# Kernel optimization log

Hardware: AMD Instinct MI355X
Metric: run time of the kernel (lower is better)

The kernel has to match this reference:

```python
import jax, jax.numpy as jnp
import numpy as np

B, N = 256, 64          # molecules, atoms per molecule
EMB = 64                # atom embedding dim
G = 64                  # n_gaussians
HID = 128               # interaction hidden
OUT = 512               # output_dim
GAUSS_WIDTH = 0.5


def setup_inputs() -> dict:
    key = jax.random.key(0)
    ks = jax.random.split(key, 10)
    atomic_nums = jax.random.randint(ks[0], (B, N), 0, 120, dtype=jnp.int64 if jax.config.x64_enabled else jnp.int32)
    coords = jax.random.normal(ks[1], (B, N, 3), dtype=jnp.float32) * 3.0
    embed_table = jax.random.normal(ks[2], (120, EMB), dtype=jnp.float32)
    # interaction: Linear(128->128), GELU, Linear(128->128); weights stored (in, out)
    W1 = jax.random.normal(ks[3], (EMB + G, HID), dtype=jnp.float32) / np.sqrt(EMB + G)
    b1 = jnp.zeros((HID,), dtype=jnp.float32)
    W2 = jax.random.normal(ks[4], (HID, HID), dtype=jnp.float32) / np.sqrt(HID)
    b2 = jnp.zeros((HID,), dtype=jnp.float32)
    # output_proj: Linear(128 -> 512)
    Wo = jax.random.normal(ks[5], (HID, OUT), dtype=jnp.float32) / np.sqrt(HID)
    bo = jnp.zeros((OUT,), dtype=jnp.float32)
    centers = jnp.linspace(0.0, 10.0, G).astype(jnp.float32)
    return {"atomic_nums": atomic_nums, "coords": coords, "embed_table": embed_table,
            "W1": W1, "b1": b1, "W2": W2, "b2": b2, "Wo": Wo, "bo": bo, "centers": centers}


def reference(atomic_nums, coords, embed_table, W1, b1, W2, b2, Wo, bo, centers):
    # per-atom embedding: [B,N,EMB]
    emb = embed_table[atomic_nums]
    # pairwise distances: [B,N,N]; guard sqrt(0) for diagonal
    diff = coords[:, :, None, :] - coords[:, None, :, :]
    sq = jnp.sum(diff * diff, axis=-1)
    pos = sq > 0
    dists = jnp.where(pos, jnp.sqrt(jnp.where(pos, sq, 1.0)), 0.0)
    # Gaussian smearing: [B,N,N,G]
    gauss = jnp.exp(-0.5 * jnp.square((dists[..., None] - centers) / GAUSS_WIDTH))
    # mean over neighbor axis j: [B,N,G]
    avg_gauss = gauss.mean(axis=2)
    feat = jnp.concatenate([emb, avg_gauss], axis=-1)  # [B,N,EMB+G]
    h = jax.nn.gelu(feat @ W1 + b1, approximate=False) @ W2 + b2  # [B,N,HID]
    mol = h.mean(axis=1)  # [B,HID]
    return mol @ Wo + bo  # [B,OUT]
```

## Files before the change

### kernel.cpp

```cpp
#include <hip/hip_runtime.h>
#include <math.h>

namespace {
constexpr int NB   = 256;
constexpr int NA   = 64;
constexpr int EMBD = 64;
constexpr int HIDD = 128;
constexpr int OUTD = 512;
constexpr int FPS  = 136;
constexpr int DSTR = 68;

typedef __attribute__((ext_vector_type(8))) short bfrag8;
typedef __attribute__((ext_vector_type(4))) float floatx4;

__device__ __forceinline__ unsigned short bf16_rne(float f) {
    unsigned u = __float_as_uint(f);
    u += 0x7fffu + ((u >> 16) & 1u);
    return (unsigned short)(u >> 16);
}

__device__ __forceinline__ float gelu_fast(float x) {
    const float ax = fabsf(x) * 0.7071067811865475f;
    const float t  = __builtin_amdgcn_rcpf(fmaf(0.3275911f, ax, 1.0f));
    float p = fmaf(1.061405429f, t, -1.453152027f);
    p = fmaf(p, t, 1.421413741f);
    p = fmaf(p, t, -0.284496736f);
    p = fmaf(p, t, 0.254829592f);
    p = p * t;
    const float e = __builtin_amdgcn_exp2f(-1.4426950408889634f * ax * ax);
    const float erfx = copysignf(fmaf(-p, e, 1.0f), x);
    const float hx   = 0.5f * x;
    return fmaf(hx, erfx, hx);
}


__global__ __launch_bounds__(1024, 1)
void mlip_fused(const int*   __restrict__ atomic_nums,
                const float* __restrict__ coords,
                const float* __restrict__ embed_table,
                const float* __restrict__ W1, const float* __restrict__ b1,
                const float* __restrict__ W2, const float* __restrict__ b2,
                const float* __restrict__ Wo, const float* __restrict__ bo,
                const float* __restrict__ centers,
                float*       __restrict__ out)
{
    const int b    = blockIdx.x;
    const int tid  = threadIdx.x;
    const int lane = tid & 63;
    const int wid  = tid >> 6;

    __shared__ float s_dist[NA * DSTR];
    __shared__ short s_w[16384];
    __shared__ short s_fhi[NA][FPS], s_flo[NA][FPS];
    __shared__ float s_mol[4][HIDD];
    __shared__ float s_molv[HIDD];

    const int wm      = wid & 3, wn = wid >> 2;
    const int lrow    = lane & 15, g4 = lane >> 4;
    const int arow    = (wm << 4) + lrow;
    const int colbase = (wn << 5) + lrow;

    const int gcol = tid & 127, kc = tid >> 7;
    const int colT = tid >> 1, kh = tid & 1;

    const int grow = tid >> 4;
    const int gch  = (tid >> 2) & 3;
    const int jq   = tid & 3;

    const float bo_r = bo[colT];
    const float b1a  = b1[colbase];
    const float b1b  = b1[colbase + 16];
    const float b2r  = b2[gcol];
    const float c0   = centers[gch << 4];

    float w1v[16];
#pragma unroll
    for (int a = 0; a < 2; ++a) {
        const int slot = (a << 10) + tid;
        const int fg = slot >> 6, ls = slot & 63;
        const int k0 = ((fg >> 3) << 5) + ((ls >> 4) << 3);
        const int n  = ((fg & 7) << 4) + (ls & 15);
        const float* src = W1 + (size_t)k0 * HIDD + n;
#pragma unroll
        for (int r = 0; r < 8; ++r) w1v[a * 8 + r] = src[(size_t)r * HIDD];
    }

    const float* cbase = coords + (size_t)b * NA * 3;
    const float cx = cbase[lane * 3 + 0];
    const float cy = cbase[lane * 3 + 1];
    const float cz = cbase[lane * 3 + 2];
    {
        const int i = tid >> 4, e4 = (tid & 15) << 2;
        const int z = atomic_nums[b * NA + i];
        const float4 ev = *(const float4*)(embed_table + (size_t)z * EMBD + e4);
        short4 h4, l4;
        const float v[4] = {ev.x, ev.y, ev.z, ev.w};
        short* hp = (short*)&h4; short* lp = (short*)&l4;
#pragma unroll
        for (int q = 0; q < 4; ++q) {
            const unsigned short h = bf16_rne(v[q]);
            hp[q] = (short)h;
            lp[q] = (short)bf16_rne(v[q] - __uint_as_float((unsigned)h << 16));
        }
        *(short4*)&s_fhi[i][e4] = h4;
        *(short4*)&s_flo[i][e4] = l4;
    }

#pragma unroll
    for (int it = 0; it < 4; ++it) {
        const int i = (wid << 2) + it;
        const float xi = __shfl(cx, i, 64);
        const float yi = __shfl(cy, i, 64);
        const float zi = __shfl(cz, i, 64);
        const float dx = xi - cx, dy = yi - cy, dz = zi - cz;
        const float sq = dx * dx + dy * dy + dz * dz;
        s_dist[i * DSTR + lane] = sq > 0.0f ? sqrtf(sq) : 0.0f;
    }

#pragma unroll
    for (int a = 0; a < 2; ++a) {
        unsigned Hu[4];
#pragma unroll
        for (int p = 0; p < 4; ++p) {
            const float x = w1v[a * 8 + 2 * p], y = w1v[a * 8 + 2 * p + 1];
            unsigned h;
            asm("v_cvt_pk_bf16_f32 %0, %1, %2" : "=v"(h) : "v"(x), "v"(y));
            Hu[p] = h;
        }
        const int slot = (a << 10) + tid;
        const int base = ((slot >> 6) << 9) + (slot & 63) * 8;
        *(uint4*)&s_w[base] = make_uint4(Hu[0], Hu[1], Hu[2], Hu[3]);
    }

    {
        constexpr float L2E   = 1.4426950408889634f;
        constexpr float DELTA = 10.0f / 63.0f;
        constexpr float K2L   = -2.0f * L2E;
        constexpr float UA    = 4.0f * DELTA * L2E;
        const float P1  = 0.95085835f,  P2  = 0.81745274f, P3  = 0.63539088f,
                    P4  = 0.44653019f,  P5  = 0.28372112f, P6  = 0.16299117f,
                    P7  = 0.08465801f,  P8  = 0.03975530f, P9  = 0.01688004f,
                    P10 = 0.00647989f,  P11 = 0.00224901f, P12 = 0.00070576f,
                    P13 = 0.00020024f,  P14 = 5.136543e-5f, P15 = 1.191313e-5f;

        float acc[16];
#pragma unroll
        for (int q = 0; q < 16; ++q) acc[q] = 0.0f;

        const float* drow = &s_dist[grow * DSTR + (jq << 4)];
#pragma unroll
        for (int j4 = 0; j4 < 4; ++j4) {
            const float4 d4 = *(const float4*)(drow + (j4 << 2));
            const float dv[4] = {d4.x, d4.y, d4.z, d4.w};
#pragma unroll
            for (int jj = 0; jj < 4; ++jj) {
                const float x = dv[jj] - c0;
                float s = __builtin_amdgcn_exp2f(K2L * x * x);
                const float r = __builtin_amdgcn_exp2f(UA * x);
                acc[0] += s;
                s *= r; acc[1]  = fmaf(s, P1,  acc[1]);
                s *= r; acc[2]  = fmaf(s, P2,  acc[2]);
                s *= r; acc[3]  = fmaf(s, P3,  acc[3]);
                s *= r; acc[4]  = fmaf(s, P4,  acc[4]);
                s *= r; acc[5]  = fmaf(s, P5,  acc[5]);
                s *= r; acc[6]  = fmaf(s, P6,  acc[6]);
                s *= r; acc[7]  = fmaf(s, P7,  acc[7]);
                s *= r; acc[8]  = fmaf(s, P8,  acc[8]);
                s *= r; acc[9]  = fmaf(s, P9,  acc[9]);
                s *= r; acc[10] = fmaf(s, P10, acc[10]);
                s *= r; acc[11] = fmaf(s, P11, acc[11]);
                s *= r; acc[12] = fmaf(s, P12, acc[12]);
                s *= r; acc[13] = fmaf(s, P13, acc[13]);
                s *= r; acc[14] = fmaf(s, P14, acc[14]);
                s *= r; acc[15] = fmaf(s, P15, acc[15]);
            }
        }
#pragma unroll
        for (int q = 0; q < 16; ++q) {
            acc[q] += __shfl_xor(acc[q], 1, 64);
            acc[q] += __shfl_xor(acc[q], 2, 64);
        }
        if (jq == 0) {
            unsigned* hp = (unsigned*)&s_fhi[grow][EMBD + (gch << 4)];
            unsigned* lp = (unsigned*)&s_flo[grow][EMBD + (gch << 4)];
#pragma unroll
            for (int q2 = 0; q2 < 8; ++q2) {
                const float v0 = acc[2 * q2]     * (1.0f / 64.0f);
                const float v1 = acc[2 * q2 + 1] * (1.0f / 64.0f);
                const unsigned h0 = bf16_rne(v0), h1 = bf16_rne(v1);
                const unsigned l0 = bf16_rne(v0 - __uint_as_float(h0 << 16));
                const unsigned l1 = bf16_rne(v1 - __uint_as_float(h1 << 16));
                hp[q2] = h0 | (h1 << 16);
                lp[q2] = l0 | (l1 << 16);
            }
        }
    }
    __syncthreads();

    float wo_a[32];
    float w2r[16];
    {
        floatx4 acc0 = {0,0,0,0}, acc1 = {0,0,0,0};
#pragma unroll
        for (int ks = 0; ks < 4; ++ks) {
            const int k0 = (ks << 5) + (g4 << 3);
            const bfrag8 ahi = *(const bfrag8*)&s_fhi[arow][k0];
            const bfrag8 alo = *(const bfrag8*)&s_flo[arow][k0];
#pragma unroll
            for (int nt = 0; nt < 2; ++nt) {
                const int base = ((((ks << 3) + (wn << 1) + nt) << 6) + lane) << 3;
                const bfrag8 bhi = *(const bfrag8*)&s_w[base];
                floatx4 a = nt ? acc1 : acc0;
                a = __builtin_amdgcn_mfma_f32_16x16x32_bf16(ahi, bhi, a, 0, 0, 0);
                a = __builtin_amdgcn_mfma_f32_16x16x32_bf16(alo, bhi, a, 0, 0, 0);
                if (nt) acc1 = a; else acc0 = a;
            }
        }

        {
            const float* wop = Wo + ((size_t)(kh << 6)) * OUTD + colT;
#pragma unroll
            for (int k = 0; k < 32; ++k) wo_a[k] = wop[(size_t)k * OUTD];
            const float* src = W2 + (size_t)(kc << 4) * HIDD + gcol;
#pragma unroll
            for (int q = 0; q < 16; ++q) w2r[q] = src[(size_t)q * HIDD];
        }

#pragma unroll
        for (int nt = 0; nt < 2; ++nt) {
            const float bb = nt ? b1b : b1a;
            const floatx4 a = nt ? acc1 : acc0;
            float s = gelu_fast(a[0] + bb) + gelu_fast(a[1] + bb)
                    + gelu_fast(a[2] + bb) + gelu_fast(a[3] + bb);
            s += __shfl_xor(s, 16, 64);
            s += __shfl_xor(s, 32, 64);
            if (lane < 16) s_mol[wm][colbase + (nt << 4)] = s;
        }
    }
    __syncthreads();

    float wo_b[32];
    {
        float acc = 0.0f;
        const int kb = kc << 4;
#pragma unroll
        for (int q = 0; q < 16; ++q) {
            const int k = kb + q;
            const float hk = (s_mol[0][k] + s_mol[1][k])
                           + (s_mol[2][k] + s_mol[3][k]);
            acc = fmaf(hk, w2r[q], acc);
        }
        s_dist[(kc << 7) + gcol] = acc;

        const float* wop = Wo + ((size_t)((kh << 6) + 32)) * OUTD + colT;
#pragma unroll
        for (int k = 0; k < 32; ++k) wo_b[k] = wop[(size_t)k * OUTD];
    }
    __syncthreads();

    if (tid < HIDD) {
        float m = 0.0f;
#pragma unroll
        for (int p = 0; p < 8; ++p) m += s_dist[(p << 7) + tid];
        s_molv[tid] = m * (1.0f / 64.0f) + b2r;
    }
    __syncthreads();

    {
        const float* mp = &s_molv[kh << 6];
        float a = 0.0f;
#pragma unroll
        for (int k = 0; k < 32; ++k) a = fmaf(mp[k], wo_a[k], a);
#pragma unroll
        for (int k = 0; k < 32; ++k) a = fmaf(mp[32 + k], wo_b[k], a);
        a += __shfl_xor(a, 1, 64);
        if (kh == 0)
            out[(size_t)b * OUTD + colT] = a + bo_r;
    }
}
}

extern "C" void kernel_launch(void* const* d_in, const int* in_sizes, int n_in,
                              void* d_out, int out_size, void* d_ws, size_t ws_size,
                              hipStream_t stream) {
    const int*   atomic_nums = (const int*)  d_in[0];
    const float* coords      = (const float*)d_in[1];
    const float* embed_table = (const float*)d_in[2];
    const float* W1          = (const float*)d_in[3];
    const float* b1          = (const float*)d_in[4];
    const float* W2          = (const float*)d_in[5];
    const float* b2          = (const float*)d_in[6];
    const float* Wo          = (const float*)d_in[7];
    const float* bo          = (const float*)d_in[8];
    const float* centers     = (const float*)d_in[9];
    float*       out         = (float*)d_out;

    mlip_fused<<<NB, 1024, 0, stream>>>(atomic_nums, coords, embed_table,
                                        W1, b1, W2, b2, Wo, bo, centers, out);
}
```

Baseline: 22.78 us.

## Drop bf16 lo-part split for features and reduce W2 GEMV via shuffles

Removes the hi/lo bf16 split of the feature matrix, so the first layer uses a single bf16 MFMA per tile instead of two and the s_flo shared buffer and its conversions go away. Separately, the W2 matvec is remapped so the 8 k-chunks of each output column sit in adjacent lanes and are reduced with xor-shuffles, which removes one shared-memory round trip and one __syncthreads. The rotated loop index is meant to spread LDS bank accesses. Feature precision drops to plain bf16, which may loosen accuracy against the fp32 reference.

```diff
diff --git a/kernel.cpp b/kernel.cpp
--- a/kernel.cpp
+++ b/kernel.cpp
@@ -51,7 +51,7 @@
 
     __shared__ float s_dist[NA * DSTR];
     __shared__ short s_w[16384];
-    __shared__ short s_fhi[NA][FPS], s_flo[NA][FPS];
+    __shared__ short s_fhi[NA][FPS];
     __shared__ float s_mol[4][HIDD];
     __shared__ float s_molv[HIDD];
 
@@ -60,7 +60,7 @@
     const int arow    = (wm << 4) + lrow;
     const int colbase = (wn << 5) + lrow;
 
-    const int gcol = tid & 127, kc = tid >> 7;
+    const int gcol = tid >> 3, kc = tid & 7;
     const int colT = tid >> 1, kh = tid & 1;
 
     const int grow = tid >> 4;
@@ -93,17 +93,12 @@
         const int i = tid >> 4, e4 = (tid & 15) << 2;
         const int z = atomic_nums[b * NA + i];
         const float4 ev = *(const float4*)(embed_table + (size_t)z * EMBD + e4);
-        short4 h4, l4;
+        short4 h4;
         const float v[4] = {ev.x, ev.y, ev.z, ev.w};
-        short* hp = (short*)&h4; short* lp = (short*)&l4;
-#pragma unroll
-        for (int q = 0; q < 4; ++q) {
-            const unsigned short h = bf16_rne(v[q]);
-            hp[q] = (short)h;
-            lp[q] = (short)bf16_rne(v[q] - __uint_as_float((unsigned)h << 16));
-        }
+        short* hp = (short*)&h4;
+#pragma unroll
+        for (int q = 0; q < 4; ++q) hp[q] = (short)bf16_rne(v[q]);
         *(short4*)&s_fhi[i][e4] = h4;
-        *(short4*)&s_flo[i][e4] = l4;
     }
 
 #pragma unroll
@@ -182,16 +177,11 @@
         }
         if (jq == 0) {
             unsigned* hp = (unsigned*)&s_fhi[grow][EMBD + (gch << 4)];
-            unsigned* lp = (unsigned*)&s_flo[grow][EMBD + (gch << 4)];
 #pragma unroll
             for (int q2 = 0; q2 < 8; ++q2) {
-                const float v0 = acc[2 * q2]     * (1.0f / 64.0f);
-                const float v1 = acc[2 * q2 + 1] * (1.0f / 64.0f);
-                const unsigned h0 = bf16_rne(v0), h1 = bf16_rne(v1);
-                const unsigned l0 = bf16_rne(v0 - __uint_as_float(h0 << 16));
-                const unsigned l1 = bf16_rne(v1 - __uint_as_float(h1 << 16));
+                const unsigned h0 = bf16_rne(acc[2 * q2]     * (1.0f / 64.0f));
+                const unsigned h1 = bf16_rne(acc[2 * q2 + 1] * (1.0f / 64.0f));
                 hp[q2] = h0 | (h1 << 16);
-                lp[q2] = l0 | (l1 << 16);
             }
         }
     }
@@ -205,15 +195,12 @@
         for (int ks = 0; ks < 4; ++ks) {
             const int k0 = (ks << 5) + (g4 << 3);
             const bfrag8 ahi = *(const bfrag8*)&s_fhi[arow][k0];
-            const bfrag8 alo = *(const bfrag8*)&s_flo[arow][k0];
 #pragma unroll
             for (int nt = 0; nt < 2; ++nt) {
                 const int base = ((((ks << 3) + (wn << 1) + nt) << 6) + lane) << 3;
                 const bfrag8 bhi = *(const bfrag8*)&s_w[base];
-                floatx4 a = nt ? acc1 : acc0;
-                a = __builtin_amdgcn_mfma_f32_16x16x32_bf16(ahi, bhi, a, 0, 0, 0);
-                a = __builtin_amdgcn_mfma_f32_16x16x32_bf16(alo, bhi, a, 0, 0, 0);
-                if (nt) acc1 = a; else acc0 = a;
+                if (nt) acc1 = __builtin_amdgcn_mfma_f32_16x16x32_bf16(ahi, bhi, acc1, 0, 0, 0);
+                else    acc0 = __builtin_amdgcn_mfma_f32_16x16x32_bf16(ahi, bhi, acc0, 0, 0, 0);
             }
         }
 
@@ -244,25 +231,21 @@
         float acc = 0.0f;
         const int kb = kc << 4;
 #pragma unroll
-        for (int q = 0; q < 16; ++q) {
+        for (int q0 = 0; q0 < 16; ++q0) {
+            const int q = (q0 + (kc << 1)) & 15;
             const int k = kb + q;
             const float hk = (s_mol[0][k] + s_mol[1][k])
                            + (s_mol[2][k] + s_mol[3][k]);
             acc = fmaf(hk, w2r[q], acc);
         }
-        s_dist[(kc << 7) + gcol] = acc;
+        acc += __shfl_xor(acc, 1, 64);
+        acc += __shfl_xor(acc, 2, 64);
+        acc += __shfl_xor(acc, 4, 64);
+        if (kc == 0) s_molv[gcol] = acc * (1.0f / 64.0f) + b2r;
 
         const float* wop = Wo + ((size_t)((kh << 6) + 32)) * OUTD + colT;
 #pragma unroll
         for (int k = 0; k < 32; ++k) wo_b[k] = wop[(size_t)k * OUTD];
-    }
-    __syncthreads();
-
-    if (tid < HIDD) {
-        float m = 0.0f;
-#pragma unroll
-        for (int p = 0; p < 8; ++p) m += s_dist[(p << 7) + tid];
-        s_molv[tid] = m * (1.0f / 64.0f) + b2r;
     }
     __syncthreads();
 
```

New measurement: 26.00 us. +14.1%, slower.
